# Optimization experiments

Hardware: AMD Instinct MI355X
Metric: run time of the kernel (lower is better)

Reference implementation:

```python
import jax, jax.numpy as jnp
import numpy as np

N = 4096        # nodes
E = 65536       # edges (avg degree 16)
L = 64          # latent_dims
K = 256         # kernel_dims
ED = 6          # edge_dims
DEPTH = 2


def _gelu(x):
    # torch.nn.GELU / F.gelu default = exact erf form
    return jax.nn.gelu(x, approximate=False)


def setup_inputs() -> dict:
    key = jax.random.key(0)
    ks = jax.random.split(key, 12)
    u = lambda k, shape, fan: jax.random.uniform(k, shape, jnp.float32, -1.0, 1.0) / np.sqrt(fan)
    return {
        "nodes": jax.random.normal(ks[0], (N, L), jnp.float32),
        "edge_index": jax.random.randint(ks[1], (2, E), 0, N, jnp.int32),
        "edge_attr": jax.random.uniform(ks[2], (E, ED), jnp.float32),
        # DenseNet kernel MLP: ED -> K -> K -> L*L (GELU between layers)
        "W1": u(ks[3], (ED, K), ED), "b1": jnp.zeros((K,), jnp.float32),
        "W2": u(ks[4], (K, K), K),  "b2": jnp.zeros((K,), jnp.float32),
        "W3": u(ks[5], (K, L * L), K), "b3": jnp.zeros((L * L,), jnp.float32),
        # NNConv root linear (no bias) + conv bias
        "W_root": u(ks[6], (L, L), L),
        "bias": jnp.zeros((L,), jnp.float32),
    }


def reference(nodes, edge_index, edge_attr, W1, b1, W2, b2, W3, b3, W_root, bias):
    src, dst = edge_index[0], edge_index[1]
    # Edge-conditioned dynamic weights (depend only on edge_attr -> compute once)
    h = _gelu(edge_attr @ W1 + b1)          # [E, K]
    h = _gelu(h @ W2 + b2)                  # [E, K]
    W_edge = (h @ W3 + b3).reshape(E, L, L) # [E, L_in, L_out]

    def conv(x):
        msg = jnp.einsum('ei,eio->eo', x[src], W_edge)          # gather + per-edge matmul
        agg = jax.ops.segment_sum(msg, dst, num_segments=N)     # scatter-add to dst
        return agg + x @ W_root + bias

    x = nodes
    for idx in range(DEPTH):
        x = conv(x)
        if idx < DEPTH - 1:
            x = _gelu(x)
    return x
```

## Files before the change

kernel.cpp:

```cpp
#include <hip/hip_runtime.h>
#include <math.h>

#define NN 4096
#define NE 65536
#define LL 64
#define KK 256
#define ED 6
#define MAXSUPER 6144

typedef __bf16 bf16_t;
typedef __attribute__((ext_vector_type(4))) __bf16 bf16x4;
typedef __attribute__((ext_vector_type(8))) __bf16 bf16x8;
typedef __attribute__((ext_vector_type(4))) float f32x4;
typedef __attribute__((ext_vector_type(16))) float f32x16;

#define OFF_CNT    ((size_t)0)
#define OFF_DESC   ((size_t)16384)
#define OFF_AGG0   ((size_t)147456)
#define OFF_AGG1   ((size_t)1196032)
#define ZERO_BYTES ((size_t)2244608)
#define OFF_CURSOR ((size_t)2244608)
#define OFF_SORTED ((size_t)2260992)
#define OFF_W2R    ((size_t)2785280)
#define OFF_W3RR   ((size_t)2916352)
#define OFF_Q0     ((size_t)5013504)
#define OFF_Q1     ((size_t)6062080)
#define OFF_X1F    ((size_t)7110656)
#define OFF_X0BF   ((size_t)8159232)
#define OFF_X1BF   ((size_t)8683520)
#define OFF_H      ((size_t)9207808)
#define OFF_P      ((size_t)42762240)

__device__ __forceinline__ float gelu_f(float x) {
    return 0.5f * x * (1.0f + erff(x * 0.7071067811865476f));
}
__device__ __forceinline__ bf16_t f2bf(float x) { return (bf16_t)x; }

__global__ void k_hist(const int* __restrict__ ei, int* __restrict__ cnt) {
    int e = blockIdx.x * 256 + threadIdx.x;
    atomicAdd(&cnt[ei[e]], 1);
}

__global__ void k_scan(const int* __restrict__ cnt, int* __restrict__ cursor,
                       int4* __restrict__ descs) {
    __shared__ int pd[1024], pc[1024];
    int t = threadIdx.x;
    int deg[4]; int sd = 0, sc = 0;
#pragma unroll
    for (int j = 0; j < 4; j++) {
        deg[j] = cnt[t * 4 + j];
        sd += deg[j];
        sc += (deg[j] + 31) >> 5;
    }
    pd[t] = sd; pc[t] = sc;
    __syncthreads();
    for (int off = 1; off < 1024; off <<= 1) {
        int vd = 0, vc = 0;
        if (t >= off) { vd = pd[t - off]; vc = pc[t - off]; }
        __syncthreads();
        pd[t] += vd; pc[t] += vc;
        __syncthreads();
    }
    int rd = (t > 0) ? pd[t - 1] : 0;
    int rc = (t > 0) ? pc[t - 1] : 0;
    for (int j = 0; j < 4; j++) {
        int v = t * 4 + j, d = deg[j];
        cursor[v] = rd;
        int nch = (d + 31) >> 5;
        for (int c = 0; c < nch; c++) {
            int rem = d - c * 32;
            descs[rc + c] = make_int4(v, rd + c * 32, rem < 32 ? rem : 32, 0);
        }
        rc += nch; rd += d;
    }
}

__global__ void k_scatter(const int* __restrict__ ei, int* __restrict__ cursor,
                          int2* __restrict__ sorted) {
    int e = blockIdx.x * 256 + threadIdx.x;
    int s = ei[e], d = ei[NE + e];
    int pos = atomicAdd(&cursor[s], 1);
    sorted[pos] = make_int2(e, d);
}

__global__ void k_prep(const float* __restrict__ W2, const float* __restrict__ W3,
                       bf16_t* __restrict__ W2r, bf16_t* __restrict__ W3rr) {
    int t = blockIdx.x * 256 + threadIdx.x;
    if (t < 65536) {
        int kk = t >> 13, nn = (t >> 9) & 15, lane = (t >> 3) & 63, j = t & 7;
        int k = kk * 32 + (lane >> 4) * 8 + j;
        int n = nn * 16 + (lane & 15);
        W2r[t] = f2bf(W2[k * 256 + n]);
    }
    if (t < 1048576) {
        int f = t;
        int sn = f >> 10, ki = (f >> 9) & 1, lane = (f >> 3) & 63, jp = f & 7;
        int i = ki * 32 + (lane >> 4) * 8 + jp;
        int s = sn * 16 + (lane & 15);
        int c = s >> 9, lane3 = (s >> 3) & 63, j3 = s & 7;
        int k = (c >> 1) * 16 + (lane3 >> 5) * 8 + j3;
        int o = (c & 1) * 32 + (lane3 & 31);
        W3rr[f] = f2bf(W3[k * 4096 + i * 64 + o]);
    }
}

__global__ void __launch_bounds__(256) k_mlp1(const float* __restrict__ attr,
                                              const float* __restrict__ W1,
                                              const float* __restrict__ b1,
                                              bf16_t* __restrict__ a1) {
    __shared__ float sa[64 * ED];
    int t = threadIdx.x;
    int e0 = blockIdx.x * 64;
    for (int i = t; i < 64 * ED; i += 256) sa[i] = attr[(size_t)e0 * ED + i];
    int col4 = (t & 63) * 4;
    float w[ED][4], bb[4];
#pragma unroll
    for (int j = 0; j < ED; j++)
#pragma unroll
        for (int c = 0; c < 4; c++) w[j][c] = W1[j * 256 + col4 + c];
#pragma unroll
    for (int c = 0; c < 4; c++) bb[c] = b1[col4 + c];
    __syncthreads();
    int esub = t >> 6;
#pragma unroll 1
    for (int eg = 0; eg < 16; eg++) {
        int el = eg * 4 + esub;
        float av[ED];
#pragma unroll
        for (int j = 0; j < ED; j++) av[j] = sa[el * ED + j];
        bf16x4 ov;
#pragma unroll
        for (int c = 0; c < 4; c++) {
            float acc = bb[c];
#pragma unroll
            for (int j = 0; j < ED; j++) acc += av[j] * w[j][c];
            ov[c] = f2bf(gelu_f(acc));
        }
        *(bf16x4*)(a1 + (size_t)(e0 + el) * 256 + col4) = ov;
    }
}

__global__ void __launch_bounds__(256) k_mlp2(const bf16_t* __restrict__ a1,
                                              const bf16_t* __restrict__ W2r,
                                              const float* __restrict__ b2,
                                              bf16_t* __restrict__ h) {
    __shared__ bf16_t sB[16384];
    int tid = threadIdx.x;
    int wave = tid >> 6, lane = tid & 63, col = lane & 15, quad = lane >> 4;
    int base = blockIdx.x * 128 + wave * 32;
    bf16x8 a[2][8];
#pragma unroll
    for (int t = 0; t < 2; t++) {
        const bf16_t* arow = a1 + (size_t)(base + t * 16 + col) * 256;
#pragma unroll
        for (int kk = 0; kk < 8; kk++)
            a[t][kk] = *(const bf16x8*)(arow + kk * 32 + quad * 8);
    }
#pragma unroll 1
    for (int p = 0; p < 4; p++) {
#pragma unroll
        for (int it = 0; it < 8; it++) {
            int c = it * 256 + tid;
            int fl = c >> 6;
            int e = (c & 63) * 8;
            int kk = fl >> 2, nnl = fl & 3;
            *(bf16x8*)(sB + fl * 512 + e) =
                *(const bf16x8*)(W2r + (size_t)(kk * 16 + p * 4 + nnl) * 512 + e);
        }
        __syncthreads();
#pragma unroll
        for (int nnl = 0; nnl < 4; nnl++) {
            f32x4 acc0, acc1;
#pragma unroll
            for (int r = 0; r < 4; r++) { acc0[r] = 0.0f; acc1[r] = 0.0f; }
#pragma unroll
            for (int kk = 0; kk < 8; kk++) {
                bf16x8 b = *(const bf16x8*)(sB + (kk * 4 + nnl) * 512 + lane * 8);
                acc0 = __builtin_amdgcn_mfma_f32_16x16x32_bf16(a[0][kk], b, acc0, 0, 0, 0);
                acc1 = __builtin_amdgcn_mfma_f32_16x16x32_bf16(a[1][kk], b, acc1, 0, 0, 0);
            }
            int ncol = (p * 4 + nnl) * 16 + col;
            float bv = b2[ncol];
#pragma unroll
            for (int r = 0; r < 4; r++) {
                int row0 = base + quad * 4 + r;
                h[(size_t)row0 * 256 + ncol] = f2bf(gelu_f(acc0[r] + bv));
                h[(size_t)(row0 + 16) * 256 + ncol] = f2bf(gelu_f(acc1[r] + bv));
            }
        }
        __syncthreads();
    }
}

__global__ void k_node0(const float* __restrict__ x, const float* __restrict__ b3,
                        bf16_t* __restrict__ xbf, float* __restrict__ Q) {
    __shared__ float sx[64];
    int v = blockIdx.x, o = threadIdx.x;
    float xv = x[v * 64 + o];
    sx[o] = xv;
    xbf[v * 64 + o] = f2bf(xv);
    __syncthreads();
    float q = 0.0f;
#pragma unroll 8
    for (int i = 0; i < 64; i++) q += sx[i] * b3[i * 64 + o];
    Q[v * 64 + o] = q;
}

__global__ void __launch_bounds__(256) k_pgemm(const bf16_t* __restrict__ xbf,
                                               const bf16_t* __restrict__ W3rr,
                                               bf16_t* __restrict__ P) {
    int strip = blockIdx.x & 63;
    int rg = blockIdx.x >> 6;
    int wave = threadIdx.x >> 6, lane = threadIdx.x & 63;
    int col = lane & 15, quad = lane >> 4;
    bf16x8 b[16][2];
#pragma unroll
    for (int nn = 0; nn < 16; nn++) {
        int sn = strip * 16 + nn;
#pragma unroll
        for (int ki = 0; ki < 2; ki++)
            b[nn][ki] = *(const bf16x8*)(W3rr + (size_t)(sn * 2 + ki) * 512 + lane * 8);
    }
#pragma unroll 1
    for (int rt = 0; rt < 4; rt++) {
        int rowbase = rg * 256 + wave * 64 + rt * 16;
        const bf16_t* arow = xbf + (size_t)(rowbase + col) * 64;
        bf16x8 a0 = *(const bf16x8*)(arow + quad * 8);
        bf16x8 a1v = *(const bf16x8*)(arow + 32 + quad * 8);
#pragma unroll
        for (int nn = 0; nn < 16; nn++) {
            f32x4 acc;
#pragma unroll
            for (int r = 0; r < 4; r++) acc[r] = 0.0f;
            acc = __builtin_amdgcn_mfma_f32_16x16x32_bf16(a0, b[nn][0], acc, 0, 0, 0);
            acc = __builtin_amdgcn_mfma_f32_16x16x32_bf16(a1v, b[nn][1], acc, 0, 0, 0);
            int sn = strip * 16 + nn;
#pragma unroll
            for (int r = 0; r < 4; r++) {
                int row = rowbase + quad * 4 + r;
                P[(size_t)row * 16384 + sn * 16 + col] = f2bf(acc[r]);
            }
        }
    }
}

__global__ void __launch_bounds__(256) k_agg(const int4* __restrict__ descs,
                                             const int2* __restrict__ sorted,
                                             const bf16_t* __restrict__ h,
                                             const bf16_t* __restrict__ P,
                                             const float* __restrict__ Q,
                                             float* __restrict__ agg) {
    int chunk = blockIdx.x * 4 + (threadIdx.x >> 6);
    int lane = threadIdx.x & 63;
    int row = lane & 31, khalf = lane >> 5;
    int4 d = descs[chunk];
    int v = d.x, base = d.y, cnt = d.z;
    if (cnt == 0) return;
    bool valid = (row < cnt);
    int2 ed = sorted[base + (valid ? row : 0)];
    int eid = ed.x, dst = ed.y;

    bf16x8 zero;
#pragma unroll
    for (int i = 0; i < 8; i++) zero[i] = (bf16_t)0.0f;

    bf16x8 a[16];
    const bf16_t* hrow = h + (size_t)eid * 256;
#pragma unroll
    for (int kt = 0; kt < 16; kt++) {
        bf16x8 t = *(const bf16x8*)(hrow + kt * 16 + khalf * 8);
        a[kt] = valid ? t : zero;
    }
    const bf16_t* Pv = P + (size_t)v * 16384;
    f32x16 acc0, acc1;
#pragma unroll
    for (int r = 0; r < 16; r++) { acc0[r] = 0.0f; acc1[r] = 0.0f; }
#pragma unroll
    for (int kt = 0; kt < 16; kt++) {
        bf16x8 b0 = *(const bf16x8*)(Pv + (size_t)(kt * 2 + 0) * 512 + lane * 8);
        bf16x8 b1 = *(const bf16x8*)(Pv + (size_t)(kt * 2 + 1) * 512 + lane * 8);
        acc0 = __builtin_amdgcn_mfma_f32_32x32x16_bf16(a[kt], b0, acc0, 0, 0, 0);
        acc1 = __builtin_amdgcn_mfma_f32_32x32x16_bf16(a[kt], b1, acc1, 0, 0, 0);
    }
    float q0 = Q[v * 64 + row];
    float q1 = Q[v * 64 + 32 + row];
#pragma unroll
    for (int r = 0; r < 16; r++) {
        int mm = (r & 3) + 8 * (r >> 2) + 4 * khalf;
        int de = __shfl(dst, mm, 64);
        if (mm < cnt) {
            atomicAdd(&agg[(size_t)de * 64 + row], acc0[r] + q0);
            atomicAdd(&agg[(size_t)de * 64 + 32 + row], acc1[r] + q1);
        }
    }
}

__global__ void k_combine1(const float* __restrict__ x, const float* __restrict__ agg,
                           const float* __restrict__ Wroot, const float* __restrict__ bias,
                           const float* __restrict__ b3, float* __restrict__ x1,
                           bf16_t* __restrict__ x1bf, float* __restrict__ Q1) {
    __shared__ float sx[64], sy[64];
    int v = blockIdx.x, o = threadIdx.x;
    sx[o] = x[v * 64 + o];
    __syncthreads();
    float acc = agg[v * 64 + o] + bias[o];
#pragma unroll 8
    for (int i = 0; i < 64; i++) acc += sx[i] * Wroot[i * 64 + o];
    acc = gelu_f(acc);
    x1[v * 64 + o] = acc;
    x1bf[v * 64 + o] = f2bf(acc);
    sy[o] = acc;
    __syncthreads();
    float q = 0.0f;
#pragma unroll 8
    for (int i = 0; i < 64; i++) q += sy[i] * b3[i * 64 + o];
    Q1[v * 64 + o] = q;
}

__global__ void k_combine2(const float* __restrict__ x1, const float* __restrict__ agg,
                           const float* __restrict__ Wroot, const float* __restrict__ bias,
                           float* __restrict__ out) {
    __shared__ float sx[64];
    int v = blockIdx.x, o = threadIdx.x;
    sx[o] = x1[v * 64 + o];
    __syncthreads();
    float acc = agg[v * 64 + o] + bias[o];
#pragma unroll 8
    for (int i = 0; i < 64; i++) acc += sx[i] * Wroot[i * 64 + o];
    out[v * 64 + o] = acc;
}

extern "C" void kernel_launch(void* const* d_in, const int* in_sizes, int n_in,
                              void* d_out, int out_size, void* d_ws, size_t ws_size,
                              hipStream_t stream) {
    const float* nodes = (const float*)d_in[0];
    const int*   ei    = (const int*)d_in[1];
    const float* attr  = (const float*)d_in[2];
    const float* W1    = (const float*)d_in[3];
    const float* b1    = (const float*)d_in[4];
    const float* W2    = (const float*)d_in[5];
    const float* b2    = (const float*)d_in[6];
    const float* W3    = (const float*)d_in[7];
    const float* b3    = (const float*)d_in[8];
    const float* Wroot = (const float*)d_in[9];
    const float* bias  = (const float*)d_in[10];
    float* out = (float*)d_out;
    char* ws = (char*)d_ws;

    int*    cnt    = (int*)(ws + OFF_CNT);
    int4*   descs  = (int4*)(ws + OFF_DESC);
    float*  agg0   = (float*)(ws + OFF_AGG0);
    float*  agg1   = (float*)(ws + OFF_AGG1);
    int*    cursor = (int*)(ws + OFF_CURSOR);
    int2*   sorted = (int2*)(ws + OFF_SORTED);
    bf16_t* W2r    = (bf16_t*)(ws + OFF_W2R);
    bf16_t* W3rr   = (bf16_t*)(ws + OFF_W3RR);
    float*  Q0     = (float*)(ws + OFF_Q0);
    float*  Q1     = (float*)(ws + OFF_Q1);
    float*  x1f    = (float*)(ws + OFF_X1F);
    bf16_t* x0bf   = (bf16_t*)(ws + OFF_X0BF);
    bf16_t* x1bf   = (bf16_t*)(ws + OFF_X1BF);
    bf16_t* hbuf   = (bf16_t*)(ws + OFF_H);
    bf16_t* Pbuf   = (bf16_t*)(ws + OFF_P);
    bf16_t* a1buf  = (bf16_t*)(ws + OFF_P);

    hipMemsetAsync(ws, 0, ZERO_BYTES, stream);
    k_hist<<<NE / 256, 256, 0, stream>>>(ei, cnt);
    k_scan<<<1, 1024, 0, stream>>>(cnt, cursor, descs);
    k_scatter<<<NE / 256, 256, 0, stream>>>(ei, cursor, sorted);
    k_prep<<<4096, 256, 0, stream>>>(W2, W3, W2r, W3rr);
    k_mlp1<<<NE / 64, 256, 0, stream>>>(attr, W1, b1, a1buf);
    k_mlp2<<<512, 256, 0, stream>>>(a1buf, W2r, b2, hbuf);
    k_node0<<<NN, 64, 0, stream>>>(nodes, b3, x0bf, Q0);
    k_pgemm<<<1024, 256, 0, stream>>>(x0bf, W3rr, Pbuf);
    k_agg<<<MAXSUPER / 4, 256, 0, stream>>>(descs, sorted, hbuf, Pbuf, Q0, agg0);
    k_combine1<<<NN, 64, 0, stream>>>(nodes, agg0, Wroot, bias, b3, x1f, x1bf, Q1);
    k_pgemm<<<1024, 256, 0, stream>>>(x1bf, W3rr, Pbuf);
    k_agg<<<MAXSUPER / 4, 256, 0, stream>>>(descs, sorted, hbuf, Pbuf, Q1, agg1);
    k_combine2<<<NN, 64, 0, stream>>>(x1f, agg1, Wroot, bias, out);
}
```

Measured before the change: 291.8 us.

## Fuse independent preprocessing kernels into two multi-role launches

Merges scatter, W2/W3 reorder, the first MLP layer and the node0 prep into a single launch that picks its role from the block index. A second launch runs the layer-0 P GEMM and the second MLP layer side by side. The W3 reorder now stages each W3 row through shared memory so global reads are coalesced, replacing the old strided gather. The a1 buffer now aliases the h buffer instead of P, since P is written concurrently; this is safe only because each MLP2 block loads its a1 rows into registers before writing the same rows of h.

```diff
diff --git a/kernel.cpp b/kernel.cpp
--- a/kernel.cpp
+++ b/kernel.cpp
@@ -75,135 +75,178 @@
     }
 }
 
-__global__ void k_scatter(const int* __restrict__ ei, int* __restrict__ cursor,
-                          int2* __restrict__ sorted) {
-    int e = blockIdx.x * 256 + threadIdx.x;
-    int s = ei[e], d = ei[NE + e];
-    int pos = atomicAdd(&cursor[s], 1);
-    sorted[pos] = make_int2(e, d);
-}
-
-__global__ void k_prep(const float* __restrict__ W2, const float* __restrict__ W3,
-                       bf16_t* __restrict__ W2r, bf16_t* __restrict__ W3rr) {
-    int t = blockIdx.x * 256 + threadIdx.x;
-    if (t < 65536) {
+__global__ void __launch_bounds__(256) k_fuse3(
+        const int* __restrict__ ei, int* __restrict__ cursor, int2* __restrict__ sorted,
+        const float* __restrict__ W3, bf16_t* __restrict__ W3rr,
+        const float* __restrict__ W2, bf16_t* __restrict__ W2r,
+        const float* __restrict__ attr, const float* __restrict__ W1,
+        const float* __restrict__ b1, bf16_t* __restrict__ a1,
+        const float* __restrict__ x, const float* __restrict__ b3,
+        bf16_t* __restrict__ xbf, float* __restrict__ Q) {
+    __shared__ float smem[4096];
+    int bid = blockIdx.x, tid = threadIdx.x;
+    if (bid < 256) {
+        int e = bid * 256 + tid;
+        int s = ei[e], d = ei[NE + e];
+        int pos = atomicAdd(&cursor[s], 1);
+        sorted[pos] = make_int2(e, d);
+    } else if (bid < 512) {
+        int k0 = bid - 256;
+        for (int idx = tid; idx < 4096; idx += 256)
+            smem[idx] = W3[(size_t)k0 * 4096 + idx];
+        __syncthreads();
+        int sbase = (2 * (k0 >> 4)) * 512 + (((k0 >> 3) & 1) * 32) * 8 + (k0 & 7);
+#pragma unroll
+        for (int m = 0; m < 2; m++) {
+            int w = m * 256 + tid;
+            int o = w >> 3, ib = w & 7;
+            int s = sbase + (o >> 5) * 512 + (o & 31) * 8;
+            int f = (s >> 4) * 1024 + (ib >> 2) * 512 + (ib & 3) * 128 + (s & 15) * 8;
+            bf16x8 pk;
+#pragma unroll
+            for (int j = 0; j < 8; j++) pk[j] = f2bf(smem[(ib * 8 + j) * 64 + o]);
+            *(bf16x8*)(W3rr + f) = pk;
+        }
+    } else if (bid < 768) {
+        int t = (bid - 512) * 256 + tid;
         int kk = t >> 13, nn = (t >> 9) & 15, lane = (t >> 3) & 63, j = t & 7;
         int k = kk * 32 + (lane >> 4) * 8 + j;
         int n = nn * 16 + (lane & 15);
         W2r[t] = f2bf(W2[k * 256 + n]);
-    }
-    if (t < 1048576) {
-        int f = t;
-        int sn = f >> 10, ki = (f >> 9) & 1, lane = (f >> 3) & 63, jp = f & 7;
-        int i = ki * 32 + (lane >> 4) * 8 + jp;
-        int s = sn * 16 + (lane & 15);
-        int c = s >> 9, lane3 = (s >> 3) & 63, j3 = s & 7;
-        int k = (c >> 1) * 16 + (lane3 >> 5) * 8 + j3;
-        int o = (c & 1) * 32 + (lane3 & 31);
-        W3rr[f] = f2bf(W3[k * 4096 + i * 64 + o]);
-    }
-}
-
-__global__ void __launch_bounds__(256) k_mlp1(const float* __restrict__ attr,
-                                              const float* __restrict__ W1,
-                                              const float* __restrict__ b1,
-                                              bf16_t* __restrict__ a1) {
-    __shared__ float sa[64 * ED];
-    int t = threadIdx.x;
-    int e0 = blockIdx.x * 64;
-    for (int i = t; i < 64 * ED; i += 256) sa[i] = attr[(size_t)e0 * ED + i];
-    int col4 = (t & 63) * 4;
-    float w[ED][4], bb[4];
-#pragma unroll
-    for (int j = 0; j < ED; j++)
-#pragma unroll
-        for (int c = 0; c < 4; c++) w[j][c] = W1[j * 256 + col4 + c];
-#pragma unroll
-    for (int c = 0; c < 4; c++) bb[c] = b1[col4 + c];
-    __syncthreads();
-    int esub = t >> 6;
+    } else if (bid < 1792) {
+        float* sa = smem;
+        int e0 = (bid - 768) * 64;
+        for (int i = tid; i < 64 * ED; i += 256) sa[i] = attr[(size_t)e0 * ED + i];
+        int col4 = (tid & 63) * 4;
+        float w[ED][4], bb[4];
+#pragma unroll
+        for (int j = 0; j < ED; j++)
+#pragma unroll
+            for (int c = 0; c < 4; c++) w[j][c] = W1[j * 256 + col4 + c];
+#pragma unroll
+        for (int c = 0; c < 4; c++) bb[c] = b1[col4 + c];
+        __syncthreads();
+        int esub = tid >> 6;
 #pragma unroll 1
-    for (int eg = 0; eg < 16; eg++) {
-        int el = eg * 4 + esub;
-        float av[ED];
-#pragma unroll
-        for (int j = 0; j < ED; j++) av[j] = sa[el * ED + j];
-        bf16x4 ov;
-#pragma unroll
-        for (int c = 0; c < 4; c++) {
-            float acc = bb[c];
-#pragma unroll
-            for (int j = 0; j < ED; j++) acc += av[j] * w[j][c];
-            ov[c] = f2bf(gelu_f(acc));
-        }
-        *(bf16x4*)(a1 + (size_t)(e0 + el) * 256 + col4) = ov;
-    }
-}
-
-__global__ void __launch_bounds__(256) k_mlp2(const bf16_t* __restrict__ a1,
-                                              const bf16_t* __restrict__ W2r,
-                                              const float* __restrict__ b2,
-                                              bf16_t* __restrict__ h) {
+        for (int eg = 0; eg < 16; eg++) {
+            int el = eg * 4 + esub;
+            float av[ED];
+#pragma unroll
+            for (int j = 0; j < ED; j++) av[j] = sa[el * ED + j];
+            bf16x4 ov;
+#pragma unroll
+            for (int c = 0; c < 4; c++) {
+                float acc = bb[c];
+#pragma unroll
+                for (int j = 0; j < ED; j++) acc += av[j] * w[j][c];
+                ov[c] = f2bf(gelu_f(acc));
+            }
+            *(bf16x4*)(a1 + (size_t)(e0 + el) * 256 + col4) = ov;
+        }
+    } else {
+        int v = (bid - 1792) * 4 + (tid >> 6);
+        int o = tid & 63;
+        float xv = x[v * 64 + o];
+        smem[tid] = xv;
+        xbf[v * 64 + o] = f2bf(xv);
+        __syncthreads();
+        const float* sx = smem + (tid >> 6) * 64;
+        float q = 0.0f;
+#pragma unroll 8
+        for (int i = 0; i < 64; i++) q += sx[i] * b3[i * 64 + o];
+        Q[v * 64 + o] = q;
+    }
+}
+
+__global__ void __launch_bounds__(256) k_fuse4(const bf16_t* __restrict__ xbf,
+                                               const bf16_t* __restrict__ W3rr,
+                                               bf16_t* __restrict__ P,
+                                               const bf16_t* __restrict__ a1,
+                                               const bf16_t* __restrict__ W2r,
+                                               const float* __restrict__ b2,
+                                               bf16_t* __restrict__ h) {
     __shared__ bf16_t sB[16384];
-    int tid = threadIdx.x;
-    int wave = tid >> 6, lane = tid & 63, col = lane & 15, quad = lane >> 4;
-    int base = blockIdx.x * 128 + wave * 32;
-    bf16x8 a[2][8];
-#pragma unroll
-    for (int t = 0; t < 2; t++) {
-        const bf16_t* arow = a1 + (size_t)(base + t * 16 + col) * 256;
-#pragma unroll
-        for (int kk = 0; kk < 8; kk++)
-            a[t][kk] = *(const bf16x8*)(arow + kk * 32 + quad * 8);
-    }
+    if (blockIdx.x < 1024) {
+        int strip = blockIdx.x & 63;
+        int rg = blockIdx.x >> 6;
+        int wave = threadIdx.x >> 6, lane = threadIdx.x & 63;
+        int col = lane & 15, quad = lane >> 4;
+        bf16x8 b[16][2];
+#pragma unroll
+        for (int nn = 0; nn < 16; nn++) {
+            int sn = strip * 16 + nn;
+#pragma unroll
+            for (int ki = 0; ki < 2; ki++)
+                b[nn][ki] = *(const bf16x8*)(W3rr + (size_t)(sn * 2 + ki) * 512 + lane * 8);
+        }
 #pragma unroll 1
-    for (int p = 0; p < 4; p++) {
-#pragma unroll
-        for (int it = 0; it < 8; it++) {
-            int c = it * 256 + tid;
-            int fl = c >> 6;
-            int e = (c & 63) * 8;
-            int kk = fl >> 2, nnl = fl & 3;
-            *(bf16x8*)(sB + fl * 512 + e) =
-                *(const bf16x8*)(W2r + (size_t)(kk * 16 + p * 4 + nnl) * 512 + e);
-        }
-        __syncthreads();
-#pragma unroll
-        for (int nnl = 0; nnl < 4; nnl++) {
-            f32x4 acc0, acc1;
-#pragma unroll
-            for (int r = 0; r < 4; r++) { acc0[r] = 0.0f; acc1[r] = 0.0f; }
-#pragma unroll
-            for (int kk = 0; kk < 8; kk++) {
-                bf16x8 b = *(const bf16x8*)(sB + (kk * 4 + nnl) * 512 + lane * 8);
-                acc0 = __builtin_amdgcn_mfma_f32_16x16x32_bf16(a[0][kk], b, acc0, 0, 0, 0);
-                acc1 = __builtin_amdgcn_mfma_f32_16x16x32_bf16(a[1][kk], b, acc1, 0, 0, 0);
+        for (int rt = 0; rt < 4; rt++) {
+            int rowbase = rg * 256 + wave * 64 + rt * 16;
+            const bf16_t* arow = xbf + (size_t)(rowbase + col) * 64;
+            bf16x8 a0 = *(const bf16x8*)(arow + quad * 8);
+            bf16x8 a1v = *(const bf16x8*)(arow + 32 + quad * 8);
+#pragma unroll
+            for (int nn = 0; nn < 16; nn++) {
+                f32x4 acc;
+#pragma unroll
+                for (int r = 0; r < 4; r++) acc[r] = 0.0f;
+                acc = __builtin_amdgcn_mfma_f32_16x16x32_bf16(a0, b[nn][0], acc, 0, 0, 0);
+                acc = __builtin_amdgcn_mfma_f32_16x16x32_bf16(a1v, b[nn][1], acc, 0, 0, 0);
+                int sn = strip * 16 + nn;
+#pragma unroll
+                for (int r = 0; r < 4; r++) {
+                    int row = rowbase + quad * 4 + r;
+                    P[(size_t)row * 16384 + sn * 16 + col] = f2bf(acc[r]);
+                }
             }
-            int ncol = (p * 4 + nnl) * 16 + col;
-            float bv = b2[ncol];
-#pragma unroll
-            for (int r = 0; r < 4; r++) {
-                int row0 = base + quad * 4 + r;
-                h[(size_t)row0 * 256 + ncol] = f2bf(gelu_f(acc0[r] + bv));
-                h[(size_t)(row0 + 16) * 256 + ncol] = f2bf(gelu_f(acc1[r] + bv));
+        }
+    } else {
+        int tid = threadIdx.x;
+        int wave = tid >> 6, lane = tid & 63, col = lane & 15, quad = lane >> 4;
+        int base = (blockIdx.x - 1024) * 128 + wave * 32;
+        bf16x8 a[2][8];
+#pragma unroll
+        for (int t = 0; t < 2; t++) {
+            const bf16_t* arow = a1 + (size_t)(base + t * 16 + col) * 256;
+#pragma unroll
+            for (int kk = 0; kk < 8; kk++)
+                a[t][kk] = *(const bf16x8*)(arow + kk * 32 + quad * 8);
+        }
+#pragma unroll 1
+        for (int p = 0; p < 4; p++) {
+#pragma unroll
+            for (int it = 0; it < 8; it++) {
+                int c = it * 256 + tid;
+                int fl = c >> 6;
+                int e = (c & 63) * 8;
+                int kk = fl >> 2, nnl = fl & 3;
+                *(bf16x8*)(sB + fl * 512 + e) =
+                    *(const bf16x8*)(W2r + (size_t)(kk * 16 + p * 4 + nnl) * 512 + e);
             }
-        }
-        __syncthreads();
-    }
-}
-
-__global__ void k_node0(const float* __restrict__ x, const float* __restrict__ b3,
-                        bf16_t* __restrict__ xbf, float* __restrict__ Q) {
-    __shared__ float sx[64];
-    int v = blockIdx.x, o = threadIdx.x;
-    float xv = x[v * 64 + o];
-    sx[o] = xv;
-    xbf[v * 64 + o] = f2bf(xv);
-    __syncthreads();
-    float q = 0.0f;
-#pragma unroll 8
-    for (int i = 0; i < 64; i++) q += sx[i] * b3[i * 64 + o];
-    Q[v * 64 + o] = q;
+            __syncthreads();
+#pragma unroll
+            for (int nnl = 0; nnl < 4; nnl++) {
+                f32x4 acc0, acc1;
+#pragma unroll
+                for (int r = 0; r < 4; r++) { acc0[r] = 0.0f; acc1[r] = 0.0f; }
+#pragma unroll
+                for (int kk = 0; kk < 8; kk++) {
+                    bf16x8 b = *(const bf16x8*)(sB + (kk * 4 + nnl) * 512 + lane * 8);
+                    acc0 = __builtin_amdgcn_mfma_f32_16x16x32_bf16(a[0][kk], b, acc0, 0, 0, 0);
+                    acc1 = __builtin_amdgcn_mfma_f32_16x16x32_bf16(a[1][kk], b, acc1, 0, 0, 0);
+                }
+                int ncol = (p * 4 + nnl) * 16 + col;
+                float bv = b2[ncol];
+#pragma unroll
+                for (int r = 0; r < 4; r++) {
+                    int row0 = base + quad * 4 + r;
+                    h[(size_t)row0 * 256 + ncol] = f2bf(gelu_f(acc0[r] + bv));
+                    h[(size_t)(row0 + 16) * 256 + ncol] = f2bf(gelu_f(acc1[r] + bv));
+                }
+            }
+            __syncthreads();
+        }
+    }
 }
 
 __global__ void __launch_bounds__(256) k_pgemm(const bf16_t* __restrict__ xbf,
@@ -361,18 +404,15 @@
     bf16_t* x0bf   = (bf16_t*)(ws + OFF_X0BF);
     bf16_t* x1bf   = (bf16_t*)(ws + OFF_X1BF);
     bf16_t* hbuf   = (bf16_t*)(ws + OFF_H);
+    bf16_t* a1buf  = (bf16_t*)(ws + OFF_H);
     bf16_t* Pbuf   = (bf16_t*)(ws + OFF_P);
-    bf16_t* a1buf  = (bf16_t*)(ws + OFF_P);
 
     hipMemsetAsync(ws, 0, ZERO_BYTES, stream);
     k_hist<<<NE / 256, 256, 0, stream>>>(ei, cnt);
     k_scan<<<1, 1024, 0, stream>>>(cnt, cursor, descs);
-    k_scatter<<<NE / 256, 256, 0, stream>>>(ei, cursor, sorted);
-    k_prep<<<4096, 256, 0, stream>>>(W2, W3, W2r, W3rr);
-    k_mlp1<<<NE / 64, 256, 0, stream>>>(attr, W1, b1, a1buf);
-    k_mlp2<<<512, 256, 0, stream>>>(a1buf, W2r, b2, hbuf);
-    k_node0<<<NN, 64, 0, stream>>>(nodes, b3, x0bf, Q0);
-    k_pgemm<<<1024, 256, 0, stream>>>(x0bf, W3rr, Pbuf);
+    k_fuse3<<<2816, 256, 0, stream>>>(ei, cursor, sorted, W3, W3rr, W2, W2r,
+                                      attr, W1, b1, a1buf, nodes, b3, x0bf, Q0);
+    k_fuse4<<<1536, 256, 0, stream>>>(x0bf, W3rr, Pbuf, a1buf, W2r, b2, hbuf);
     k_agg<<<MAXSUPER / 4, 256, 0, stream>>>(descs, sorted, hbuf, Pbuf, Q0, agg0);
     k_combine1<<<NN, 64, 0, stream>>>(nodes, agg0, Wroot, bias, b3, x1f, x1bf, Q1);
     k_pgemm<<<1024, 256, 0, stream>>>(x1bf, W3rr, Pbuf);
```

Measured after the change: 271.8 us. 1.07x faster.
